# Kernel tuning notes

Hardware: AMD Instinct MI355X
Metric: run time of the kernel (lower is better)

## Reference

```python
import jax, jax.numpy as jnp
import numpy as np
import math

B, L, HID, NH = 4, 4096, 1024, 8
DH = HID // NH
THETA = 10000.0


def _rope_tables(seq_len, dh):
    half = dh // 2
    inv_freq = 1.0 / (THETA ** (jnp.arange(half, dtype=jnp.float32) / half))
    freqs = jnp.arange(seq_len, dtype=jnp.float32)[:, None] * inv_freq[None, :]  # [L, half]
    return jnp.cos(freqs), jnp.sin(freqs)


def _apply_rope(x, cos, sin):
    # x: [B,H,L,D], D even
    half = x.shape[-1] // 2
    x1, x2 = x[..., :half], x[..., half:2 * half]
    c = cos[None, None]
    s = sin[None, None]
    return jnp.concatenate([x1 * c - x2 * s, x1 * s + x2 * c], axis=-1)


def setup_inputs() -> dict:
    key = jax.random.key(0)
    ks = jax.random.split(key, 9)
    def xav(k, sh):
        lim = math.sqrt(6.0 / (sh[0] + sh[1]))
        return jax.random.uniform(k, sh, jnp.float32, -lim, lim)
    return {
        "x": jax.random.normal(ks[0], (B, L, HID), jnp.float32),
        "norm_w": jnp.ones((HID,), jnp.float32),
        "Wq": xav(ks[1], (HID, HID)),
        "Wk": xav(ks[2], (HID, HID)),
        "Wv": xav(ks[3], (HID, HID)),
        "Wbeta": xav(ks[4], (NH, HID)),
        "bbeta": jnp.full((NH,), 2.0, jnp.float32),  # retention-favoring init
        "Wig": xav(ks[5], (NH, HID)),
        "big": jnp.zeros((NH,), jnp.float32),
        "Wog": xav(ks[6], (NH, HID)),
        "bog": jnp.zeros((NH,), jnp.float32),
        "Wout": xav(ks[7], (HID, HID)),
        "bout": jnp.zeros((HID,), jnp.float32),
    }


def reference(x, norm_w, Wq, Wk, Wv, Wbeta, bbeta, Wig, big, Wog, bog, Wout, bout):
    Bq, Lq, _ = x.shape
    # RMSNorm (no mean subtraction)
    h = x * jax.lax.rsqrt(jnp.mean(x * x, axis=-1, keepdims=True) + 1e-6) * norm_w
    # q/k/v projections (torch Linear: h @ W.T), split heads -> [B,H,L,Dh]
    def heads(W):
        return jnp.einsum('bld,ed->ble', h, W).reshape(Bq, Lq, NH, DH).transpose(0, 2, 1, 3)
    q, k, v = heads(Wq), heads(Wk), heads(Wv)
    cos, sin = _rope_tables(Lq, DH)
    q = _apply_rope(q, cos, sin)
    k = _apply_rope(k, cos, sin)
    # token-conditional gates -> [B,H,L]
    def gate(W, b):
        return jax.nn.sigmoid(jnp.einsum('bld,hd->blh', h, W) + b).transpose(0, 2, 1)
    beta, ig, og = gate(Wbeta, bbeta), gate(Wig, big), gate(Wog, bog)
    scale = 1.0 / math.sqrt(DH)
    # time-major for the sequential delta-rule scan
    qT = q.transpose(2, 0, 1, 3)  # [L,B,H,D]
    kT = k.transpose(2, 0, 1, 3)
    vT = v.transpose(2, 0, 1, 3)
    fT = beta.transpose(2, 0, 1)  # [L,B,H]
    gT = ig.transpose(2, 0, 1)
    oT = og.transpose(2, 0, 1)
    M0 = jnp.zeros((Bq, NH, DH, DH), x.dtype)
    def step(M, inp):
        q_t, k_t, v_t, f_t, g_t, o_t = inp
        M = M * f_t[..., None, None] + (g_t[..., None, None] * scale) * (k_t[..., :, None] * v_t[..., None, :])
        y_t = jnp.einsum('bhd,bhde->bhe', q_t, M) * o_t[..., None]
        return M, y_t
    _, yT = jax.lax.scan(step, M0, (qT, kT, vT, fT, gT, oT))  # yT: [L,B,H,D]
    y = yT.transpose(1, 0, 2, 3).reshape(Bq, Lq, HID)  # b l (h d)
    return jnp.einsum('bld,ed->ble', y, Wout) + bout
```

## Files before the change

### kernel.cpp

```cpp
#include <hip/hip_runtime.h>
#include <hip/hip_bf16.h>

#define BQ 4
#define LQ 4096
#define HID 1024
#define NHEAD 8
#define DHEAD 128
#define MROWS (BQ * LQ)
#define CCH 64
#define NCH (LQ / CCH)

typedef __bf16 bf16x8 __attribute__((ext_vector_type(8)));
typedef float f32x4 __attribute__((ext_vector_type(4)));

__device__ __forceinline__ float bf2f(unsigned short u) {
    return __uint_as_float(((unsigned int)u) << 16);
}
__device__ __forceinline__ unsigned short f2us(float f) {
    __hip_bfloat16 b = __float2bfloat16(f);
    return *reinterpret_cast<unsigned short*>(&b);
}
__device__ __forceinline__ float loadAny(const void* p, size_t i, bool isf) {
    return isf ? ((const float*)p)[i] : bf2f(((const unsigned short*)p)[i]);
}

__global__ void detect_kernel(const void* x, int* flag) {
    const unsigned short* u = (const unsigned short*)x;
    int t = threadIdx.x;
    int cnt = 0;
#pragma unroll
    for (int s = 0; s < 64; ++s) {
        unsigned short v = u[2 * (t * 64 + s)];
        int e = (v >> 7) & 0xFF;
        cnt += (e >= 0x8A || (e != 0 && e <= 0x6E)) ? 1 : 0;
    }
#pragma unroll
    for (int m = 1; m < 64; m <<= 1) cnt += __shfl_xor(cnt, m);
    if (t == 0) *flag = (cnt > 1024) ? 1 : 0;
}

__global__ __launch_bounds__(256) void cvt_w4_kernel(
    const void* Wq, const void* Wk, const void* Wv, const void* Wout,
    unsigned short* dq, unsigned short* dk, unsigned short* dv, unsigned short* dout,
    float* __restrict__ cosT, float* __restrict__ sinT,
    const int* flagp) {
    if (blockIdx.y == 4) {
        int idx = blockIdx.x * 256 + threadIdx.x;
        int l = idx >> 6, i = idx & 63;
        float invf = powf(10000.0f, -(float)i * (1.0f / 64.0f));
        float fr = (float)l * invf;
        cosT[idx] = cosf(fr);
        sinT[idx] = sinf(fr);
        return;
    }
    const bool isf = (*flagp != 0);
    const void* s;
    unsigned short* d;
    switch (blockIdx.y) {
        case 0: s = Wq; d = dq; break;
        case 1: s = Wk; d = dk; break;
        case 2: s = Wv; d = dv; break;
        default: s = Wout; d = dout; break;
    }
    size_t i = ((size_t)blockIdx.x * 256 + threadIdx.x) * 4;
#pragma unroll
    for (int r = 0; r < 4; ++r) d[i + r] = f2us(loadAny(s, i + r, isf));
}

__global__ __launch_bounds__(256) void cvt_small_kernel(
    const void* Wbeta, const void* Wig, const void* Wog,
    const void* bbeta, const void* big, const void* bog, const void* bout,
    unsigned short* dWb, unsigned short* dWi, unsigned short* dWo,
    float* dbb, float* dbi, float* dbo, float* dbout,
    const int* flagp) {
    const bool isf = (*flagp != 0);
    int gid = blockIdx.x * 256 + threadIdx.x;
    if (gid < 24576) {
        int seg = gid >> 13, off = gid & 8191;
        const void* s = (seg == 0) ? Wbeta : (seg == 1) ? Wig : Wog;
        unsigned short* d = (seg == 0) ? dWb : (seg == 1) ? dWi : dWo;
        d[off] = f2us(loadAny(s, off, isf));
    } else {
        int j = gid - 24576;
        if (j < 8) dbb[j] = loadAny(bbeta, j, isf);
        else if (j < 16) dbi[j - 8] = loadAny(big, j - 8, isf);
        else if (j < 24) dbo[j - 16] = loadAny(bog, j - 16, isf);
        else if (j < 24 + 1024) dbout[j - 24] = loadAny(bout, j - 24, isf);
    }
}

__global__ __launch_bounds__(256) void rmsnorm_gates_kernel(
    const void* __restrict__ xin, const void* __restrict__ win,
    __hip_bfloat16* __restrict__ h, const int* __restrict__ flagp,
    const __hip_bfloat16* __restrict__ Wbeta, const float* __restrict__ bbeta,
    const __hip_bfloat16* __restrict__ Wig, const float* __restrict__ big,
    const __hip_bfloat16* __restrict__ Wog, const float* __restrict__ bog,
    float* __restrict__ fT, float* __restrict__ gT, float* __restrict__ oT) {
    const bool isf = (*flagp != 0);
    const int row = blockIdx.x;
    const int tid = threadIdx.x;
    const int lane = tid & 63, wave = tid >> 6;
    const int b = row >> 12, l = row & (LQ - 1);
    const size_t base = (size_t)row * HID;
    float x0, x1, x2, x3;
    if (isf) {
        float4 u = ((const float4*)((const float*)xin + base))[tid];
        x0 = u.x; x1 = u.y; x2 = u.z; x3 = u.w;
    } else {
        ushort4 u = ((const ushort4*)((const unsigned short*)xin + base))[tid];
        x0 = bf2f(u.x); x1 = bf2f(u.y); x2 = bf2f(u.z); x3 = bf2f(u.w);
    }
    float ss = x0 * x0 + x1 * x1 + x2 * x2 + x3 * x3;
#pragma unroll
    for (int m = 1; m < 64; m <<= 1) ss += __shfl_xor(ss, m);
    __shared__ float wsum[4];
    if (lane == 0) wsum[wave] = ss;
    __syncthreads();
    float tot = wsum[0] + wsum[1] + wsum[2] + wsum[3];
    float inv = rsqrtf(tot * (1.0f / HID) + 1e-6f);
    float w0, w1, w2, w3;
    if (isf) {
        float4 u = ((const float4*)win)[tid];
        w0 = u.x; w1 = u.y; w2 = u.z; w3 = u.w;
    } else {
        ushort4 u = ((const ushort4*)win)[tid];
        w0 = bf2f(u.x); w1 = bf2f(u.y); w2 = bf2f(u.z); w3 = bf2f(u.w);
    }
    float h0 = x0 * inv * w0, h1 = x1 * inv * w1, h2 = x2 * inv * w2, h3 = x3 * inv * w3;
    __hip_bfloat16* ho = h + base + tid * 4;
    ho[0] = __float2bfloat16(h0);
    ho[1] = __float2bfloat16(h1);
    ho[2] = __float2bfloat16(h2);
    ho[3] = __float2bfloat16(h3);
    float p[24];
#pragma unroll
    for (int g = 0; g < 24; ++g) {
        const __hip_bfloat16* wr = (g < 8) ? (Wbeta + g * HID)
                                 : (g < 16) ? (Wig + (g - 8) * HID)
                                            : (Wog + (g - 16) * HID);
        const unsigned short* wp = (const unsigned short*)wr + tid * 4;
        ushort4 wu = *(const ushort4*)wp;
        p[g] = h0 * bf2f(wu.x) + h1 * bf2f(wu.y) + h2 * bf2f(wu.z) + h3 * bf2f(wu.w);
    }
#pragma unroll
    for (int m = 1; m < 64; m <<= 1) {
#pragma unroll
        for (int g = 0; g < 24; ++g) p[g] += __shfl_xor(p[g], m);
    }
    __shared__ float part[4][24];
    if (lane == 0) {
#pragma unroll
        for (int g = 0; g < 24; ++g) part[wave][g] = p[g];
    }
    __syncthreads();
    if (tid < 24) {
        int g = tid;
        float s = part[0][g] + part[1][g] + part[2][g] + part[3][g];
        float bb = (g < 8) ? bbeta[g] : (g < 16) ? big[g - 8] : bog[g - 16];
        s += bb;
        s = 1.0f / (1.0f + expf(-s));
        int hh = (g < 8) ? g : (g < 16) ? g - 8 : g - 16;
        float* dst = (g < 8) ? fT : (g < 16) ? gT : oT;
        dst[((size_t)(b * NHEAD + hh)) * LQ + l] = s;
    }
}

__global__ __launch_bounds__(256) void gemm_qkv(const __hip_bfloat16* __restrict__ A,
                                                const unsigned short* __restrict__ Wqc,
                                                const unsigned short* __restrict__ Wkc,
                                                const unsigned short* __restrict__ Wvc,
                                                unsigned short* __restrict__ qb,
                                                unsigned short* __restrict__ kb,
                                                unsigned short* __restrict__ vb) {
    __shared__ unsigned short As[128 * 32];
    __shared__ unsigned short Bs[128 * 32];
    const int sel = blockIdx.y >> 3;
    const __hip_bfloat16* W = (const __hip_bfloat16*)(sel == 0 ? Wqc : sel == 1 ? Wkc : Wvc);
    unsigned short* C = (sel == 0) ? qb : (sel == 1) ? kb : vb;
    const int tid = threadIdx.x;
    const int lane = tid & 63, wave = tid >> 6;
    const int m0 = blockIdx.x * 128, n0 = (blockIdx.y & 7) * 128;
    const int wm = (wave & 1) * 64, wn = (wave >> 1) * 64;
    const int lm = lane & 15, lq = lane >> 4;
    f32x4 acc[4][4] = {};
    const int c0 = tid, c1 = tid + 256;
    const int r0 = c0 >> 2, o0 = (c0 & 3) * 8;
    const int r1 = c1 >> 2, o1 = (c1 & 3) * 8;
    for (int k0 = 0; k0 < HID; k0 += 32) {
        __builtin_amdgcn_global_load_lds(
            (const __attribute__((address_space(1))) void*)(A + (size_t)(m0 + r0) * HID + k0 + o0),
            (__attribute__((address_space(3))) void*)(As + c0 * 8), 16, 0, 0);
        __builtin_amdgcn_global_load_lds(
            (const __attribute__((address_space(1))) void*)(A + (size_t)(m0 + r1) * HID + k0 + o1),
            (__attribute__((address_space(3))) void*)(As + c1 * 8), 16, 0, 0);
        __builtin_amdgcn_global_load_lds(
            (const __attribute__((address_space(1))) void*)(W + (size_t)(n0 + r0) * HID + k0 + o0),
            (__attribute__((address_space(3))) void*)(Bs + c0 * 8), 16, 0, 0);
        __builtin_amdgcn_global_load_lds(
            (const __attribute__((address_space(1))) void*)(W + (size_t)(n0 + r1) * HID + k0 + o1),
            (__attribute__((address_space(3))) void*)(Bs + c1 * 8), 16, 0, 0);
        __syncthreads();
        bf16x8 af[4], bfr[4];
#pragma unroll
        for (int i = 0; i < 4; ++i)
            af[i] = *(const bf16x8*)(const void*)(As + (wm + i * 16 + lm) * 32 + lq * 8);
#pragma unroll
        for (int j = 0; j < 4; ++j)
            bfr[j] = *(const bf16x8*)(const void*)(Bs + (wn + j * 16 + lm) * 32 + lq * 8);
#pragma unroll
        for (int i = 0; i < 4; ++i)
#pragma unroll
            for (int j = 0; j < 4; ++j)
                acc[i][j] = __builtin_amdgcn_mfma_f32_16x16x32_bf16(af[i], bfr[j], acc[i][j], 0, 0, 0);
        __syncthreads();
    }
#pragma unroll
    for (int i = 0; i < 4; ++i)
#pragma unroll
        for (int j = 0; j < 4; ++j) {
            int col = n0 + wn + j * 16 + lm;
#pragma unroll
            for (int r = 0; r < 4; ++r) {
                int rowg = m0 + wm + i * 16 + lq * 4 + r;
                C[(size_t)rowg * HID + col] = f2us(acc[i][j][r]);
            }
        }
}

__global__ __launch_bounds__(256) void gemm_bt(const __hip_bfloat16* __restrict__ A,
                                               const __hip_bfloat16* __restrict__ W,
                                               const float* __restrict__ bias,
                                               void* __restrict__ C,
                                               const int* __restrict__ flagp) {
    __shared__ unsigned short As[128 * 32];
    __shared__ unsigned short Bs[128 * 32];
    const bool f32out = (*flagp != 0);
    const int tid = threadIdx.x;
    const int lane = tid & 63, wave = tid >> 6;
    const int m0 = blockIdx.x * 128, n0 = blockIdx.y * 128;
    const int wm = (wave & 1) * 64, wn = (wave >> 1) * 64;
    const int lm = lane & 15, lq = lane >> 4;
    f32x4 acc[4][4] = {};
    const int c0 = tid, c1 = tid + 256;
    const int r0 = c0 >> 2, o0 = (c0 & 3) * 8;
    const int r1 = c1 >> 2, o1 = (c1 & 3) * 8;
    for (int k0 = 0; k0 < HID; k0 += 32) {
        __builtin_amdgcn_global_load_lds(
            (const __attribute__((address_space(1))) void*)(A + (size_t)(m0 + r0) * HID + k0 + o0),
            (__attribute__((address_space(3))) void*)(As + c0 * 8), 16, 0, 0);
        __builtin_amdgcn_global_load_lds(
            (const __attribute__((address_space(1))) void*)(A + (size_t)(m0 + r1) * HID + k0 + o1),
            (__attribute__((address_space(3))) void*)(As + c1 * 8), 16, 0, 0);
        __builtin_amdgcn_global_load_lds(
            (const __attribute__((address_space(1))) void*)(W + (size_t)(n0 + r0) * HID + k0 + o0),
            (__attribute__((address_space(3))) void*)(Bs + c0 * 8), 16, 0, 0);
        __builtin_amdgcn_global_load_lds(
            (const __attribute__((address_space(1))) void*)(W + (size_t)(n0 + r1) * HID + k0 + o1),
            (__attribute__((address_space(3))) void*)(Bs + c1 * 8), 16, 0, 0);
        __syncthreads();
        bf16x8 af[4], bfr[4];
#pragma unroll
        for (int i = 0; i < 4; ++i)
            af[i] = *(const bf16x8*)(const void*)(As + (wm + i * 16 + lm) * 32 + lq * 8);
#pragma unroll
        for (int j = 0; j < 4; ++j)
            bfr[j] = *(const bf16x8*)(const void*)(Bs + (wn + j * 16 + lm) * 32 + lq * 8);
#pragma unroll
        for (int i = 0; i < 4; ++i)
#pragma unroll
            for (int j = 0; j < 4; ++j)
                acc[i][j] = __builtin_amdgcn_mfma_f32_16x16x32_bf16(af[i], bfr[j], acc[i][j], 0, 0, 0);
        __syncthreads();
    }
#pragma unroll
    for (int i = 0; i < 4; ++i)
#pragma unroll
        for (int j = 0; j < 4; ++j) {
            int col = n0 + wn + j * 16 + lm;
            float bv = bias[col];
#pragma unroll
            for (int r = 0; r < 4; ++r) {
                int rowg = m0 + wm + i * 16 + lq * 4 + r;
                size_t idx = (size_t)rowg * HID + col;
                float val = acc[i][j][r] + bv;
                if (f32out) ((float*)C)[idx] = val;
                else ((__hip_bfloat16*)C)[idx] = __float2bfloat16(val);
            }
        }
}

__global__ __launch_bounds__(256) void intra_kernel(
    unsigned short* __restrict__ qg, const unsigned short* __restrict__ kg,
    const unsigned short* __restrict__ vg,
    const float* __restrict__ fT, const float* __restrict__ gT, const float* __restrict__ oT,
    const float* __restrict__ cosT, const float* __restrict__ sinT,
    __hip_bfloat16* __restrict__ yb,
    unsigned short* __restrict__ ktg, float* __restrict__ cdecG) {
    const int chunk = blockIdx.x;
    const int bh = blockIdx.y;
    const int b = bh >> 3, hh = bh & 7;
    const int t0 = chunk * CCH;
    const int tid = threadIdx.x;
    const int lane = tid & 63, wave = tid >> 6;
    const int lm = lane & 15, lq = lane >> 4;
    __shared__ unsigned short Kr[64 * 136];
    __shared__ unsigned short Vt[128 * 72];
    __shared__ unsigned short Sp[64 * 72];
    __shared__ float Lp[64], aS[64], osh[64], w2s[64], qscs[64];

    if (tid < 64) {
        float f = fT[(size_t)bh * LQ + t0 + tid];
        float g = gT[(size_t)bh * LQ + t0 + tid];
        osh[tid] = oT[(size_t)bh * LQ + t0 + tid];
        float lf = __logf(f);
#pragma unroll
        for (int off = 1; off < 64; off <<= 1) {
            float v = __shfl_up(lf, off);
            if (lane >= off) lf += v;
        }
        float tot = __shfl(lf, 63);
        Lp[tid] = lf;
        aS[tid] = g * 0.08838834764831845f;
        w2s[tid] = __expf(tot - lf) * (g * 0.08838834764831845f);
        qscs[tid] = __expf(lf);
        if (tid == 63) cdecG[bh * NCH + chunk] = __expf(lf);
    }
    __syncthreads();

    bf16x8 af[4];
    {
        const int jr = 16 * wave + lm;
        const int gt = t0 + jr;
        const size_t qbase = ((size_t)(b * LQ + gt)) * HID + hh * DHEAD;
        uint4 qraw[4];
#pragma unroll
        for (int ks = 0; ks < 4; ++ks)
            qraw[ks] = *(const uint4*)(qg + qbase + ks * 32 + lq * 8);
        const unsigned short* q0 = (const unsigned short*)&qraw[0];
        const unsigned short* q1 = (const unsigned short*)&qraw[1];
        const unsigned short* q2 = (const unsigned short*)&qraw[2];
        const unsigned short* q3 = (const unsigned short*)&qraw[3];
        const float sc = qscs[jr];
        __align__(16) unsigned short fr[4][8];
        __align__(16) unsigned short qo[4][8];
#pragma unroll
        for (int u = 0; u < 8; ++u) {
            int i = lq * 8 + u;
            int i2 = 32 + lq * 8 + u;
            float c0 = cosT[gt * 64 + i], s0 = sinT[gt * 64 + i];
            float c1 = cosT[gt * 64 + i2], s1 = sinT[gt * 64 + i2];
            float a = bf2f(q0[u]), bq = bf2f(q2[u]);
            float rc = a * c0 - bq * s0, rs = a * s0 + bq * c0;
            fr[0][u] = f2us(rc); fr[2][u] = f2us(rs);
            qo[0][u] = f2us(rc * sc); qo[2][u] = f2us(rs * sc);
            float a1 = bf2f(q1[u]), bq1 = bf2f(q3[u]);
            float rc1 = a1 * c1 - bq1 * s1, rs1 = a1 * s1 + bq1 * c1;
            fr[1][u] = f2us(rc1); fr[3][u] = f2us(rs1);
            qo[1][u] = f2us(rc1 * sc); qo[3][u] = f2us(rs1 * sc);
        }
#pragma unroll
        for (int ks = 0; ks < 4; ++ks) {
            af[ks] = *(const bf16x8*)fr[ks];
            *(uint4*)(qg + qbase + ks * 32 + lq * 8) = *(const uint4*)qo[ks];
        }
    }
#pragma unroll
    for (int r = 0; r < 16; ++r) {
        int pid = r * 256 + tid;
        int t = pid >> 6, i = pid & 63;
        int gt = t0 + t;
        size_t gidx = ((size_t)(b * LQ + gt)) * HID + hh * DHEAD + i;
        float c = cosT[gt * 64 + i], s = sinT[gt * 64 + i];
        float k1 = bf2f(kg[gidx]), k2 = bf2f(kg[gidx + 64]);
        Kr[t * 136 + i] = f2us(k1 * c - k2 * s);
        Kr[t * 136 + i + 64] = f2us(k1 * s + k2 * c);
    }
#pragma unroll
    for (int r = 0; r < 32; ++r) {
        int lin = r * 256 + tid;
        int sI = lin >> 7, e = lin & 127;
        float val = bf2f(vg[((size_t)(b * LQ + t0 + sI)) * HID + hh * DHEAD + e]);
        Vt[e * 72 + sI] = f2us(val);
    }
    __syncthreads();

    f32x4 sacc[4] = {};
#pragma unroll
    for (int ks = 0; ks < 4; ++ks) {
#pragma unroll
        for (int nt = 0; nt < 4; ++nt) {
            bf16x8 bf = *(const bf16x8*)(const void*)(Kr + (nt * 16 + lm) * 136 + ks * 32 + lq * 8);
            sacc[nt] = __builtin_amdgcn_mfma_f32_16x16x32_bf16(af[ks], bf, sacc[nt], 0, 0, 0);
        }
    }
#pragma unroll
    for (int nt = 0; nt < 4; ++nt) {
#pragma unroll
        for (int r = 0; r < 4; ++r) {
            int j = 16 * wave + lq * 4 + r;
            int s = nt * 16 + lm;
            float v = 0.0f;
            if (j >= s) v = sacc[nt][r] * __expf(Lp[j] - Lp[s]) * aS[s];
            Sp[j * 72 + s] = f2us(v);
        }
    }
    {
        unsigned short* krec = ktg + ((size_t)(bh * NCH + chunk)) * 8192;
#pragma unroll
        for (int r = 0; r < 2; ++r) {
            int lin16 = r * 256 + tid;
            int ks = lin16 >> 8;
            int d = (lin16 & 255) >> 1;
            int cc0 = (lin16 & 1) * 16;
            __align__(16) unsigned short out[16];
#pragma unroll
            for (int u = 0; u < 16; ++u) {
                int s = ks * 32 + cc0 + u;
                out[u] = f2us(w2s[s] * bf2f(Kr[s * 136 + d]));
            }
            uint4* dst = (uint4*)(krec + (size_t)lin16 * 16);
            dst[0] = *(const uint4*)(out);
            dst[1] = *(const uint4*)(out + 8);
        }
    }
    __syncthreads();

    f32x4 ya[8] = {};
#pragma unroll
    for (int ks = 0; ks < 2; ++ks) {
        bf16x8 afs = *(const bf16x8*)(const void*)(Sp + (16 * wave + lm) * 72 + ks * 32 + lq * 8);
#pragma unroll
        for (int nt = 0; nt < 8; ++nt) {
            bf16x8 bf = *(const bf16x8*)(const void*)(Vt + (nt * 16 + lm) * 72 + ks * 32 + lq * 8);
            ya[nt] = __builtin_amdgcn_mfma_f32_16x16x32_bf16(afs, bf, ya[nt], 0, 0, 0);
        }
    }
#pragma unroll
    for (int nt = 0; nt < 8; ++nt) {
#pragma unroll
        for (int r = 0; r < 4; ++r) {
            int j = 16 * wave + lq * 4 + r;
            int e = nt * 16 + lm;
            size_t row = (size_t)(b * LQ + t0 + j);
            yb[row * HID + hh * DHEAD + e] = __float2bfloat16(osh[j] * ya[nt][r]);
        }
    }
}

__global__ __launch_bounds__(256) void inter_kernel(
    const unsigned short* __restrict__ qs,
    const unsigned short* __restrict__ ktg,
    const unsigned short* __restrict__ vg,
    const float* __restrict__ oT, const float* __restrict__ cdecG,
    unsigned short* __restrict__ yb) {
    const int bh = blockIdx.x;
    const int esplit = blockIdx.y;
    const int e0 = esplit * 16;
    const int b = bh >> 3, hh = bh & 7;
    const int tid = threadIdx.x;
    const int lane = tid & 63, wave = tid >> 6;
    const int lm = lane & 15, lq = lane >> 4;
    __shared__ __align__(16) unsigned short Qsl[2][8192];
    __shared__ __align__(16) unsigned short Ktl[2][8192];
    __shared__ __align__(16) unsigned short Vtl[2][1024];
    __shared__ __align__(16) float Ml[2][16 * 132];

    for (int i = tid; i < 16 * 132; i += 256) Ml[0][i] = 0.0f;

    const int jrow = tid >> 2;
    const int qcol = (tid & 3) * 8;
    {
        const unsigned short* qrow =
            qs + ((size_t)(b * LQ + jrow)) * HID + hh * DHEAD + qcol;
#pragma unroll
        for (int ks = 0; ks < 4; ++ks)
            __builtin_amdgcn_global_load_lds(
                (const __attribute__((address_space(1))) void*)(qrow + ks * 32),
                (__attribute__((address_space(3))) void*)(&Qsl[0][ks * 2048 + tid * 8]),
                16, 0, 0);
        const unsigned short* kbase = ktg + ((size_t)(bh * NCH)) * 8192 + tid * 8;
#pragma unroll
        for (int i = 0; i < 4; ++i)
            __builtin_amdgcn_global_load_lds(
                (const __attribute__((address_space(1))) void*)(kbase + i * 2048),
                (__attribute__((address_space(3))) void*)(&Ktl[0][i * 2048 + tid * 8]),
                16, 0, 0);
#pragma unroll
        for (int r = 0; r < 4; ++r) {
            int lin = r * 256 + tid;
            int s = lin >> 4, e = lin & 15;
            float val = bf2f(vg[((size_t)(b * LQ + s)) * HID + hh * DHEAD + e0 + e]);
            Vtl[0][(s >> 5) * 512 + e * 32 + (s & 31)] = f2us(val);
        }
    }

    for (int c = 0; c < NCH; ++c) {
        const int cur = c & 1, nxt = cur ^ 1;
        const int t0 = c * CCH;
        __syncthreads();
        if (c + 1 < NCH) {
            const int t0n = t0 + CCH;
            const unsigned short* qrow =
                qs + ((size_t)(b * LQ + t0n + jrow)) * HID + hh * DHEAD + qcol;
#pragma unroll
            for (int ks = 0; ks < 4; ++ks)
                __builtin_amdgcn_global_load_lds(
                    (const __attribute__((address_space(1))) void*)(qrow + ks * 32),
                    (__attribute__((address_space(3))) void*)(&Qsl[nxt][ks * 2048 + tid * 8]),
                    16, 0, 0);
            const unsigned short* kbase = ktg + ((size_t)(bh * NCH + c + 1)) * 8192 + tid * 8;
#pragma unroll
            for (int i = 0; i < 4; ++i)
                __builtin_amdgcn_global_load_lds(
                    (const __attribute__((address_space(1))) void*)(kbase + i * 2048),
                    (__attribute__((address_space(3))) void*)(&Ktl[nxt][i * 2048 + tid * 8]),
                    16, 0, 0);
        }
        size_t yidx[4];
        unsigned short prevy[4];
        float osv[4];
#pragma unroll
        for (int r = 0; r < 4; ++r) {
            int j = 16 * wave + lq * 4 + r;
            yidx[r] = ((size_t)(b * LQ + t0 + j)) * HID + hh * DHEAD + e0 + lm;
            prevy[r] = yb[yidx[r]];
            osv[r] = oT[(size_t)bh * LQ + t0 + j];
        }
        const float cd = cdecG[bh * NCH + c];
        f32x4 uacc[2] = {};
#pragma unroll
        for (int ks = 0; ks < 2; ++ks) {
            bf16x8 bfv = *(const bf16x8*)(const void*)(&Vtl[cur][ks * 512 + lm * 32 + lq * 8]);
#pragma unroll
            for (int mt = 0; mt < 2; ++mt) {
                bf16x8 af = *(const bf16x8*)(const void*)(
                    &Ktl[cur][ks * 4096 + (32 * wave + 16 * mt + lm) * 32 + lq * 8]);
                uacc[mt] = __builtin_amdgcn_mfma_f32_16x16x32_bf16(af, bfv, uacc[mt], 0, 0, 0);
            }
        }
        f32x4 yacc = {};
#pragma unroll
        for (int ks = 0; ks < 4; ++ks) {
            bf16x8 af = *(const bf16x8*)(const void*)(
                &Qsl[cur][ks * 2048 + (16 * wave + lm) * 32 + lq * 8]);
            float4 m0 = *(const float4*)(const void*)(&Ml[cur][lm * 132 + ks * 32 + lq * 8]);
            float4 m1 = *(const float4*)(const void*)(&Ml[cur][lm * 132 + ks * 32 + lq * 8 + 4]);
            __align__(16) unsigned short tmp[8];
            tmp[0] = f2us(m0.x); tmp[1] = f2us(m0.y); tmp[2] = f2us(m0.z); tmp[3] = f2us(m0.w);
            tmp[4] = f2us(m1.x); tmp[5] = f2us(m1.y); tmp[6] = f2us(m1.z); tmp[7] = f2us(m1.w);
            bf16x8 bfm = *(const bf16x8*)tmp;
            yacc = __builtin_amdgcn_mfma_f32_16x16x32_bf16(af, bfm, yacc, 0, 0, 0);
        }
#pragma unroll
        for (int r = 0; r < 4; ++r)
            yb[yidx[r]] = f2us(bf2f(prevy[r]) + osv[r] * yacc[r]);
        if (c + 1 < NCH) {
            const int t0n = t0 + CCH;
#pragma unroll
            for (int r = 0; r < 4; ++r) {
                int lin = r * 256 + tid;
                int s = lin >> 4, e = lin & 15;
                float val = bf2f(vg[((size_t)(b * LQ + t0n + s)) * HID + hh * DHEAD + e0 + e]);
                Vtl[nxt][(s >> 5) * 512 + e * 32 + (s & 31)] = f2us(val);
            }
        }
#pragma unroll
        for (int mt = 0; mt < 2; ++mt)
#pragma unroll
            for (int r = 0; r < 4; ++r) {
                int d = 32 * wave + 16 * mt + lq * 4 + r;
                Ml[nxt][lm * 132 + d] = cd * Ml[cur][lm * 132 + d] + uacc[mt][r];
            }
    }
}

extern "C" void kernel_launch(void* const* d_in, const int* in_sizes, int n_in,
                              void* d_out, int out_size, void* d_ws, size_t ws_size,
                              hipStream_t stream) {
    const void* x      = d_in[0];
    const void* norm_w = d_in[1];
    const void* Wq     = d_in[2];
    const void* Wk     = d_in[3];
    const void* Wv     = d_in[4];
    const void* Wbeta  = d_in[5];
    const void* bbeta  = d_in[6];
    const void* Wig    = d_in[7];
    const void* big    = d_in[8];
    const void* Wog    = d_in[9];
    const void* bog    = d_in[10];
    const void* Wout   = d_in[11];
    const void* bout   = d_in[12];

    char* ws = (char*)d_ws;
    const size_t KB = 1024, MB = 1024 * 1024;
    int*   flag    = (int*)(ws + 0);
    float* bbeta_c = (float*)(ws + 1 * KB);
    float* big_c   = (float*)(ws + 1 * KB + 32);
    float* bog_c   = (float*)(ws + 1 * KB + 64);
    float* bout_c  = (float*)(ws + 4 * KB);
    float* cdecG   = (float*)(ws + 16 * KB);
    unsigned short* Wbeta_c = (unsigned short*)(ws + 64 * KB);
    unsigned short* Wig_c   = (unsigned short*)(ws + 96 * KB);
    unsigned short* Wog_c   = (unsigned short*)(ws + 128 * KB);
    float* fT   = (float*)(ws + 1 * MB);
    float* gT   = (float*)(ws + 1 * MB + 512 * KB);
    float* oT   = (float*)(ws + 2 * MB);
    float* cosT = (float*)(ws + 2 * MB + 512 * KB);
    float* sinT = (float*)(ws + 3 * MB + 512 * KB);
    unsigned short* Wq_c   = (unsigned short*)(ws + 5 * MB);
    unsigned short* Wk_c   = (unsigned short*)(ws + 7 * MB);
    unsigned short* Wv_c   = (unsigned short*)(ws + 9 * MB);
    unsigned short* Wout_c = (unsigned short*)(ws + 11 * MB);
    __hip_bfloat16* h  = (__hip_bfloat16*)(ws + 16 * MB);
    unsigned short* ktg = (unsigned short*)(ws + 16 * MB);
    unsigned short* qb = (unsigned short*)(ws + 48 * MB);
    unsigned short* kb = (unsigned short*)(ws + 80 * MB);
    unsigned short* vb = (unsigned short*)(ws + 112 * MB);
    __hip_bfloat16* yb = (__hip_bfloat16*)(ws + 144 * MB);

    detect_kernel<<<1, 64, 0, stream>>>(x, flag);
    cvt_w4_kernel<<<dim3(1024, 5), 256, 0, stream>>>(Wq, Wk, Wv, Wout,
                                                     Wq_c, Wk_c, Wv_c, Wout_c,
                                                     cosT, sinT, flag);
    cvt_small_kernel<<<101, 256, 0, stream>>>(Wbeta, Wig, Wog, bbeta, big, bog, bout,
                                              Wbeta_c, Wig_c, Wog_c,
                                              bbeta_c, big_c, bog_c, bout_c, flag);
    rmsnorm_gates_kernel<<<MROWS, 256, 0, stream>>>(
        x, norm_w, h, flag,
        (const __hip_bfloat16*)Wbeta_c, bbeta_c,
        (const __hip_bfloat16*)Wig_c, big_c,
        (const __hip_bfloat16*)Wog_c, bog_c, fT, gT, oT);

    gemm_qkv<<<dim3(MROWS / 128, 24), 256, 0, stream>>>(h, Wq_c, Wk_c, Wv_c, qb, kb, vb);

    intra_kernel<<<dim3(NCH, 32), 256, 0, stream>>>(qb, kb, vb, fT, gT, oT, cosT, sinT,
                                                    (__hip_bfloat16*)yb, ktg, cdecG);
    inter_kernel<<<dim3(32, 8), 256, 0, stream>>>(qb, ktg, vb, oT, cdecG,
                                                  (unsigned short*)yb);

    gemm_bt<<<dim3(MROWS / 128, HID / 128), 256, 0, stream>>>(
        (const __hip_bfloat16*)yb, (const __hip_bfloat16*)Wout_c, bout_c, d_out, flag);
}
```

Baseline: 542.7 us.

## Rewrite QKV and output GEMMs with 256x256 tiles, double-buffered swizzled LDS

Both projection GEMMs move from 128x128 tiles with 256 threads and a k-step of 32 to 256x256 tiles with 512 threads and a k-step of 64. LDS is double-buffered and filled asynchronously with global_load_lds, with an XOR swizzle to avoid bank conflicts. Explicit waitcnt, sched_barrier and setprio calls interleave the prefetch of the next k-tile with the MFMA phases. The aim is more data reuse per tile and hiding of global load latency. In exchange, the larger LDS footprint (128 KB per block) and accumulator count lower occupancy, and there are fewer blocks in the grid (768 for QKV, 256 for the output projection).

```diff
diff --git a/kernel.cpp b/kernel.cpp
--- a/kernel.cpp
+++ b/kernel.cpp
@@ -9,6 +9,7 @@
 #define MROWS (BQ * LQ)
 #define CCH 64
 #define NCH (LQ / CCH)
+#define GNT 16
 
 typedef __bf16 bf16x8 __attribute__((ext_vector_type(8)));
 typedef float f32x4 __attribute__((ext_vector_type(4)));
@@ -165,128 +166,178 @@
     }
 }
 
-__global__ __launch_bounds__(256) void gemm_qkv(const __hip_bfloat16* __restrict__ A,
+__device__ __forceinline__ void g256_stage_half(const unsigned short* __restrict__ src,
+                                                unsigned short* lds, int tid) {
+#pragma unroll
+    for (int l = 0; l < 2; ++l) {
+        int L = l * 512 + tid;
+        int r = L >> 3, g = L & 7;
+        int gs = g ^ (r & 7);
+        __builtin_amdgcn_global_load_lds(
+            (const __attribute__((address_space(1))) void*)(src + (size_t)r * HID + gs * 8),
+            (__attribute__((address_space(3))) void*)(lds + L * 8), 16, 0, 0);
+    }
+}
+
+#define G256_SEAL() __builtin_amdgcn_sched_barrier(0)
+#define G256_BARRIER()            \
+    do {                          \
+        G256_SEAL();              \
+        __builtin_amdgcn_s_barrier(); \
+        G256_SEAL();              \
+    } while (0)
+
+__device__ __forceinline__ void g256_core(const unsigned short* __restrict__ A,
+                                          const unsigned short* __restrict__ W,
+                                          unsigned short* As, unsigned short* Bs,
+                                          int m0, int tid, f32x4 (&acc)[8][4]) {
+    const int lane = tid & 63, wid = tid >> 6;
+    const int wr = wid >> 2, wc = wid & 3;
+    const int lm = lane & 15, lq = lane >> 4;
+    g256_stage_half(A + (size_t)m0 * HID, As, tid);
+    g256_stage_half(W, Bs, tid);
+    g256_stage_half(W + (size_t)128 * HID, Bs + 8192, tid);
+    g256_stage_half(A + (size_t)(m0 + 128) * HID, As + 8192, tid);
+    G256_SEAL();
+    asm volatile("s_waitcnt vmcnt(0)" ::: "memory");
+    G256_BARRIER();
+    for (int t = 0; t < GNT; ++t) {
+        unsigned short* Ac = As + (t & 1) * 16384;
+        unsigned short* Bc = Bs + (t & 1) * 16384;
+        unsigned short* An = As + ((t & 1) ^ 1) * 16384;
+        unsigned short* Bn = Bs + ((t & 1) ^ 1) * 16384;
+        const int kn = (t + 1) * 64;
+        const bool pf = (t + 1 < GNT);
+#pragma unroll
+        for (int ph = 0; ph < 4; ++ph) {
+            const int mq = ph >> 1, nq = ph & 1;
+            bf16x8 af[4][2], bfr[2][2];
+#pragma unroll
+            for (int i = 0; i < 4; ++i) {
+                const int row = mq * 128 + wr * 64 + i * 16 + lm;
+#pragma unroll
+                for (int kk = 0; kk < 2; ++kk) {
+                    const int gsw = (kk * 4 + lq) ^ (lm & 7);
+                    af[i][kk] = *(const bf16x8*)(const void*)(Ac + row * 64 + gsw * 8);
+                }
+            }
+#pragma unroll
+            for (int j = 0; j < 2; ++j) {
+                const int row = nq * 128 + wc * 32 + j * 16 + lm;
+#pragma unroll
+                for (int kk = 0; kk < 2; ++kk) {
+                    const int gsw = (kk * 4 + lq) ^ (lm & 7);
+                    bfr[j][kk] = *(const bf16x8*)(const void*)(Bc + row * 64 + gsw * 8);
+                }
+            }
+            if (pf) {
+                if (ph == 0) g256_stage_half(A + (size_t)m0 * HID + kn, An, tid);
+                if (ph == 1) g256_stage_half(W + kn, Bn, tid);
+                if (ph == 2) g256_stage_half(W + (size_t)128 * HID + kn, Bn + 8192, tid);
+                if (ph == 3) g256_stage_half(A + (size_t)(m0 + 128) * HID + kn, An + 8192, tid);
+            }
+            G256_BARRIER();
+            asm volatile("s_waitcnt lgkmcnt(0)" ::: "memory");
+            G256_SEAL();
+            __builtin_amdgcn_s_setprio(1);
+#pragma unroll
+            for (int i = 0; i < 4; ++i)
+#pragma unroll
+                for (int j = 0; j < 2; ++j)
+#pragma unroll
+                    for (int kk = 0; kk < 2; ++kk)
+                        acc[mq * 4 + i][nq * 2 + j] = __builtin_amdgcn_mfma_f32_16x16x32_bf16(
+                            af[i][kk], bfr[j][kk], acc[mq * 4 + i][nq * 2 + j], 0, 0, 0);
+            __builtin_amdgcn_s_setprio(0);
+            G256_SEAL();
+            if (ph == 0) {
+                if (pf) asm volatile("s_waitcnt vmcnt(4)" ::: "memory");
+                else    asm volatile("s_waitcnt vmcnt(2)" ::: "memory");
+            } else if (ph == 1) {
+                if (pf) asm volatile("s_waitcnt vmcnt(4)" ::: "memory");
+                else    asm volatile("s_waitcnt vmcnt(0)" ::: "memory");
+            } else if (ph == 3) {
+                if (pf) asm volatile("s_waitcnt vmcnt(4)" ::: "memory");
+            }
+            G256_BARRIER();
+        }
+    }
+}
+
+__global__ __launch_bounds__(512) void gemm_qkv(const __hip_bfloat16* __restrict__ A,
                                                 const unsigned short* __restrict__ Wqc,
                                                 const unsigned short* __restrict__ Wkc,
                                                 const unsigned short* __restrict__ Wvc,
                                                 unsigned short* __restrict__ qb,
                                                 unsigned short* __restrict__ kb,
                                                 unsigned short* __restrict__ vb) {
-    __shared__ unsigned short As[128 * 32];
-    __shared__ unsigned short Bs[128 * 32];
-    const int sel = blockIdx.y >> 3;
-    const __hip_bfloat16* W = (const __hip_bfloat16*)(sel == 0 ? Wqc : sel == 1 ? Wkc : Wvc);
+    __shared__ __align__(16) unsigned short As[2 * 16384];
+    __shared__ __align__(16) unsigned short Bs[2 * 16384];
+    const int nblk = blockIdx.y;
+    const int sel = nblk >> 2;
+    const int nl0 = (nblk & 3) * 256;
+    const unsigned short* W = (sel == 0 ? Wqc : sel == 1 ? Wkc : Wvc) + (size_t)nl0 * HID;
     unsigned short* C = (sel == 0) ? qb : (sel == 1) ? kb : vb;
     const int tid = threadIdx.x;
-    const int lane = tid & 63, wave = tid >> 6;
-    const int m0 = blockIdx.x * 128, n0 = (blockIdx.y & 7) * 128;
-    const int wm = (wave & 1) * 64, wn = (wave >> 1) * 64;
+    const int lane = tid & 63, wid = tid >> 6;
+    const int wr = wid >> 2, wc = wid & 3;
     const int lm = lane & 15, lq = lane >> 4;
-    f32x4 acc[4][4] = {};
-    const int c0 = tid, c1 = tid + 256;
-    const int r0 = c0 >> 2, o0 = (c0 & 3) * 8;
-    const int r1 = c1 >> 2, o1 = (c1 & 3) * 8;
-    for (int k0 = 0; k0 < HID; k0 += 32) {
-        __builtin_amdgcn_global_load_lds(
-            (const __attribute__((address_space(1))) void*)(A + (size_t)(m0 + r0) * HID + k0 + o0),
-            (__attribute__((address_space(3))) void*)(As + c0 * 8), 16, 0, 0);
-        __builtin_amdgcn_global_load_lds(
-            (const __attribute__((address_space(1))) void*)(A + (size_t)(m0 + r1) * HID + k0 + o1),
-            (__attribute__((address_space(3))) void*)(As + c1 * 8), 16, 0, 0);
-        __builtin_amdgcn_global_load_lds(
-            (const __attribute__((address_space(1))) void*)(W + (size_t)(n0 + r0) * HID + k0 + o0),
-            (__attribute__((address_space(3))) void*)(Bs + c0 * 8), 16, 0, 0);
-        __builtin_amdgcn_global_load_lds(
-            (const __attribute__((address_space(1))) void*)(W + (size_t)(n0 + r1) * HID + k0 + o1),
-            (__attribute__((address_space(3))) void*)(Bs + c1 * 8), 16, 0, 0);
-        __syncthreads();
-        bf16x8 af[4], bfr[4];
+    const int m0 = blockIdx.x * 256;
+    f32x4 acc[8][4] = {};
+    g256_core((const unsigned short*)A, W, As, Bs, m0, tid, acc);
+#pragma unroll
+    for (int mq = 0; mq < 2; ++mq)
 #pragma unroll
         for (int i = 0; i < 4; ++i)
-            af[i] = *(const bf16x8*)(const void*)(As + (wm + i * 16 + lm) * 32 + lq * 8);
-#pragma unroll
-        for (int j = 0; j < 4; ++j)
-            bfr[j] = *(const bf16x8*)(const void*)(Bs + (wn + j * 16 + lm) * 32 + lq * 8);
-#pragma unroll
-        for (int i = 0; i < 4; ++i)
-#pragma unroll
-            for (int j = 0; j < 4; ++j)
-                acc[i][j] = __builtin_amdgcn_mfma_f32_16x16x32_bf16(af[i], bfr[j], acc[i][j], 0, 0, 0);
-        __syncthreads();
-    }
-#pragma unroll
-    for (int i = 0; i < 4; ++i)
-#pragma unroll
-        for (int j = 0; j < 4; ++j) {
-            int col = n0 + wn + j * 16 + lm;
-#pragma unroll
-            for (int r = 0; r < 4; ++r) {
-                int rowg = m0 + wm + i * 16 + lq * 4 + r;
-                C[(size_t)rowg * HID + col] = f2us(acc[i][j][r]);
-            }
-        }
-}
-
-__global__ __launch_bounds__(256) void gemm_bt(const __hip_bfloat16* __restrict__ A,
+#pragma unroll
+            for (int nq = 0; nq < 2; ++nq)
+#pragma unroll
+                for (int j = 0; j < 2; ++j) {
+                    const int col = nl0 + nq * 128 + wc * 32 + j * 16 + lm;
+#pragma unroll
+                    for (int r = 0; r < 4; ++r) {
+                        const int rowg = m0 + mq * 128 + wr * 64 + i * 16 + lq * 4 + r;
+                        C[(size_t)rowg * HID + col] = f2us(acc[mq * 4 + i][nq * 2 + j][r]);
+                    }
+                }
+}
+
+__global__ __launch_bounds__(512) void gemm_bt(const __hip_bfloat16* __restrict__ A,
                                                const __hip_bfloat16* __restrict__ W,
                                                const float* __restrict__ bias,
                                                void* __restrict__ C,
                                                const int* __restrict__ flagp) {
-    __shared__ unsigned short As[128 * 32];
-    __shared__ unsigned short Bs[128 * 32];
+    __shared__ __align__(16) unsigned short As[2 * 16384];
+    __shared__ __align__(16) unsigned short Bs[2 * 16384];
     const bool f32out = (*flagp != 0);
     const int tid = threadIdx.x;
-    const int lane = tid & 63, wave = tid >> 6;
-    const int m0 = blockIdx.x * 128, n0 = blockIdx.y * 128;
-    const int wm = (wave & 1) * 64, wn = (wave >> 1) * 64;
+    const int lane = tid & 63, wid = tid >> 6;
+    const int wr = wid >> 2, wc = wid & 3;
     const int lm = lane & 15, lq = lane >> 4;
-    f32x4 acc[4][4] = {};
-    const int c0 = tid, c1 = tid + 256;
-    const int r0 = c0 >> 2, o0 = (c0 & 3) * 8;
-    const int r1 = c1 >> 2, o1 = (c1 & 3) * 8;
-    for (int k0 = 0; k0 < HID; k0 += 32) {
-        __builtin_amdgcn_global_load_lds(
-            (const __attribute__((address_space(1))) void*)(A + (size_t)(m0 + r0) * HID + k0 + o0),
-            (__attribute__((address_space(3))) void*)(As + c0 * 8), 16, 0, 0);
-        __builtin_amdgcn_global_load_lds(
-            (const __attribute__((address_space(1))) void*)(A + (size_t)(m0 + r1) * HID + k0 + o1),
-            (__attribute__((address_space(3))) void*)(As + c1 * 8), 16, 0, 0);
-        __builtin_amdgcn_global_load_lds(
-            (const __attribute__((address_space(1))) void*)(W + (size_t)(n0 + r0) * HID + k0 + o0),
-            (__attribute__((address_space(3))) void*)(Bs + c0 * 8), 16, 0, 0);
-        __builtin_amdgcn_global_load_lds(
-            (const __attribute__((address_space(1))) void*)(W + (size_t)(n0 + r1) * HID + k0 + o1),
-            (__attribute__((address_space(3))) void*)(Bs + c1 * 8), 16, 0, 0);
-        __syncthreads();
-        bf16x8 af[4], bfr[4];
+    const int m0 = blockIdx.x * 256;
+    const int nl0 = blockIdx.y * 256;
+    f32x4 acc[8][4] = {};
+    g256_core((const unsigned short*)A, (const unsigned short*)W + (size_t)nl0 * HID,
+              As, Bs, m0, tid, acc);
+#pragma unroll
+    for (int mq = 0; mq < 2; ++mq)
 #pragma unroll
         for (int i = 0; i < 4; ++i)
-            af[i] = *(const bf16x8*)(const void*)(As + (wm + i * 16 + lm) * 32 + lq * 8);
-#pragma unroll
-        for (int j = 0; j < 4; ++j)
-            bfr[j] = *(const bf16x8*)(const void*)(Bs + (wn + j * 16 + lm) * 32 + lq * 8);
-#pragma unroll
-        for (int i = 0; i < 4; ++i)
-#pragma unroll
-            for (int j = 0; j < 4; ++j)
-                acc[i][j] = __builtin_amdgcn_mfma_f32_16x16x32_bf16(af[i], bfr[j], acc[i][j], 0, 0, 0);
-        __syncthreads();
-    }
-#pragma unroll
-    for (int i = 0; i < 4; ++i)
-#pragma unroll
-        for (int j = 0; j < 4; ++j) {
-            int col = n0 + wn + j * 16 + lm;
-            float bv = bias[col];
-#pragma unroll
-            for (int r = 0; r < 4; ++r) {
-                int rowg = m0 + wm + i * 16 + lq * 4 + r;
-                size_t idx = (size_t)rowg * HID + col;
-                float val = acc[i][j][r] + bv;
-                if (f32out) ((float*)C)[idx] = val;
-                else ((__hip_bfloat16*)C)[idx] = __float2bfloat16(val);
-            }
-        }
+#pragma unroll
+            for (int nq = 0; nq < 2; ++nq)
+#pragma unroll
+                for (int j = 0; j < 2; ++j) {
+                    const int col = nl0 + nq * 128 + wc * 32 + j * 16 + lm;
+                    const float bv = bias[col];
+#pragma unroll
+                    for (int r = 0; r < 4; ++r) {
+                        const int rowg = m0 + mq * 128 + wr * 64 + i * 16 + lq * 4 + r;
+                        const size_t idx = (size_t)rowg * HID + col;
+                        const float val = acc[mq * 4 + i][nq * 2 + j][r] + bv;
+                        if (f32out) ((float*)C)[idx] = val;
+                        else ((__hip_bfloat16*)C)[idx] = __float2bfloat16(val);
+                    }
+                }
 }
 
 __global__ __launch_bounds__(256) void intra_kernel(
@@ -631,13 +682,13 @@
         (const __hip_bfloat16*)Wig_c, big_c,
         (const __hip_bfloat16*)Wog_c, bog_c, fT, gT, oT);
 
-    gemm_qkv<<<dim3(MROWS / 128, 24), 256, 0, stream>>>(h, Wq_c, Wk_c, Wv_c, qb, kb, vb);
+    gemm_qkv<<<dim3(MROWS / 256, 12), 512, 0, stream>>>(h, Wq_c, Wk_c, Wv_c, qb, kb, vb);
 
     intra_kernel<<<dim3(NCH, 32), 256, 0, stream>>>(qb, kb, vb, fT, gT, oT, cosT, sinT,
                                                     (__hip_bfloat16*)yb, ktg, cdecG);
     inter_kernel<<<dim3(32, 8), 256, 0, stream>>>(qb, ktg, vb, oT, cdecG,
                                                   (unsigned short*)yb);
 
-    gemm_bt<<<dim3(MROWS / 128, HID / 128), 256, 0, stream>>>(
+    gemm_bt<<<dim3(MROWS / 256, HID / 256), 512, 0, stream>>>(
         (const __hip_bfloat16*)yb, (const __hip_bfloat16*)Wout_c, bout_c, d_out, flag);
 }
```

After: 534.8 us. About the same (-1.4%).
